# Kernel tuning notes

Hardware: AMD Instinct MI355X
Metric: run time of the kernel (lower is better)

## Reference

```python
import jax, jax.numpy as jnp
import numpy as np

BATCH = 128
SITES = 256      # input_dim, number of MPS input cores
BOND = 64        # bond dimension D
FEAT = 2         # feature_dim
OUT = 10         # output_dim


def setup_inputs() -> dict:
    key = jax.random.key(0)
    k1, k2, k3, k4, k5 = jax.random.split(key, 5)
    # forward input: [batch, input_dim, feature_dim], values in [0,1) like a feature map
    input_data = jax.random.uniform(k1, (BATCH, SITES, FEAT), dtype=jnp.float32)
    # InputRegion core tensor, bond_str 'slri' -> [sites, D, D, feat]
    # small random perturbation; identity bias (use_bias=True, fixed_bias) added in forward
    cores = 0.01 * jax.random.normal(k2, (SITES, BOND, BOND, FEAT), dtype=jnp.float32)
    # OutputSite core, bond_str 'olr' -> [output_dim, D, D]
    out_core = 0.01 * jax.random.normal(k3, (OUT, BOND, BOND), dtype=jnp.float32)
    # boundary (edge) vectors for open boundary conditions
    left_vec = jax.random.normal(k4, (BOND,), dtype=jnp.float32) / np.sqrt(BOND)
    right_vec = jax.random.normal(k5, (BOND,), dtype=jnp.float32) / np.sqrt(BOND)
    return {"input_data": input_data, "cores": cores, "out_core": out_core,
            "left_vec": left_vec, "right_vec": right_vec}


def _chain_matmul(mats):
    """Log-depth product of a chain of matrices. mats: [b, s, D, D] -> [b, D, D].
    Product is ordered: mats[:,0] @ mats[:,1] @ ... @ mats[:,s-1]."""
    b, s, d, _ = mats.shape
    while mats.shape[1] > 1:
        n = mats.shape[1]
        if n % 2 == 1:  # pad with identity so length is even
            eye = jnp.broadcast_to(jnp.eye(d, dtype=mats.dtype), (b, 1, d, d))
            mats = jnp.concatenate([mats, eye], axis=1)
        mats = jnp.matmul(mats[:, 0::2], mats[:, 1::2])
    return mats[:, 0]


def reference(input_data, cores, out_core, left_vec, right_vec):
    # InputRegion.forward: contract each core with its per-site feature vector
    # 'slri,bsi->bslr', then add identity bias matrix (use_bias=True)
    mats = jnp.einsum('slri,bsi->bslr', cores, input_data)
    mats = mats + jnp.eye(BOND, dtype=mats.dtype)  # bias_mat = eye, broadcast over b,s

    # split the chain around the (central) output site, reduce each side
    half = SITES // 2
    left_prod = _chain_matmul(mats[:, :half])    # [b, D, D]
    right_prod = _chain_matmul(mats[:, half:])   # [b, D, D]

    # open-boundary contraction: lvec . Lprod . out_core . Rprod . rvec -> [b, out]
    v = jnp.einsum('l,blr->br', left_vec, left_prod)        # [b, D]
    v = jnp.einsum('bl,olr->bor', v, out_core)              # [b, out, D]
    v = jnp.einsum('bol,blr->bor', v, right_prod)           # [b, out, D]
    logits = jnp.einsum('bor,r->bo', v, right_vec)          # [b, out]
    return logits
```

## Files before the change

kernel.cpp:

```cpp
#include <hip/hip_runtime.h>

#define BOND   64
#define SITES  256
#define HALF   128
#define NBATCH 128
#define OUTD   10

#define P1_OFF   1048576
#define VEC_OFF  2097152
#define SITE_F4  2048
#define LPITCH   132

typedef __attribute__((ext_vector_type(4))) float f32x4;
#define AS1 __attribute__((address_space(1)))
#define AS3 __attribute__((address_space(3)))

__global__ void __launch_bounds__(256)
mps_pack_kernel(const float* __restrict__ cores, float* __restrict__ P) {
  __shared__ __align__(16) float ld[64 * LPITCH];
  const int s = (int)blockIdx.x;
  const int t = (int)threadIdx.x;
  const float4* src = (const float4*)(cores + (size_t)s * 8192);
  #pragma unroll
  for (int k = 0; k < 8; ++k) {
    const int m = t + 256 * k;
    const int row = m >> 5;
    const int c4  = m & 31;
    *(float4*)&ld[row * LPITCH + c4 * 4] = src[m];
  }
  __syncthreads();
  const bool right = s >= HALF;
  const int step = right ? (SITES - 1 - s) : s;
  float4* out = (float4*)(P + (right ? P1_OFF : 0)) + (size_t)step * SITE_F4;
  #pragma unroll
  for (int k = 0; k < 8; ++k) {
    const int m = t + 256 * k;
    const int g = m >> 6;
    const int j = m & 63;
    float4 v;
    if (!right) {
      const float2 a  = *(const float2*)&ld[(2 * g) * LPITCH + 2 * j];
      const float2 b2 = *(const float2*)&ld[(2 * g + 1) * LPITCH + 2 * j];
      v = make_float4(a.x, a.y, b2.x, b2.y);
    } else {
      v = *(const float4*)&ld[j * LPITCH + 4 * g];
    }
    out[m] = v;
  }
}

__device__ __forceinline__ void gload_lds16(const float* g, float* l) {
  __builtin_amdgcn_global_load_lds((const AS1 void*)g, (AS3 void*)l, 16, 0, 0);
}

__global__ void __launch_bounds__(192, 1)
mps_chain_kernel(const float* __restrict__ input,
                 const float* __restrict__ P,
                 const float* __restrict__ lvec,
                 const float* __restrict__ rvec,
                 float* __restrict__ vout) {
  __shared__ __align__(16) float buf0[8192];
  __shared__ __align__(16) float buf1[8192];
  __shared__ __align__(16) float buf2[8192];
  __shared__ __align__(16) float vb[2][68];
  __shared__ __align__(16) float xsh[2][HALF][2];

  const int t    = (int)threadIdx.x;
  const int side = (int)blockIdx.x & 1;
  const int pair = (int)blockIdx.x >> 1;
  const int b0   = 2 * pair;

  if (t < 64) {
    const int lane = t;
    const float* gl = P + (side ? P1_OFF : 0) + lane * 4;
    float* sA = buf0;
    float* sB = buf1;
    float* sC = buf2;
#define STAGEL(LDST, STEPI)                                                  \
    {                                                                        \
      const float* gs = gl + (size_t)(STEPI) * 8192;                         \
      _Pragma("unroll")                                                      \
      for (int k = 0; k < 32; ++k)                                           \
        gload_lds16(gs + k * 256, (LDST) + k * 256);                         \
    }
    STAGEL(sA, 0);
    STAGEL(sB, 1);
    for (int i = 0; i < HALF; ++i) {
      asm volatile("s_waitcnt vmcnt(32)" ::: "memory");
      __builtin_amdgcn_s_barrier();
      const int inx = (i + 2 < HALF) ? i + 2 : HALF - 1;
      STAGEL(sC, inx);
      float* tmp = sA; sA = sB; sB = sC; sC = tmp;
    }
#undef STAGEL
  } else {
    const int tc   = t - 64;
    const int wc   = tc >> 6;
    const int lane = tc & 63;
    const int jcol = (lane >> 1) + 32 * wc;
    const int bs   = lane & 1;

    if (wc == 0) {
      #pragma unroll
      for (int bi = 0; bi < 2; ++bi) {
        const float4 g = ((const float4*)(input + (size_t)(b0 + bi) * SITES * 2 +
                                          side * HALF * 2))[lane];
        float* xw = &xsh[bi][0][0];
        if (!side) {
          ((float4*)xw)[lane] = g;
        } else {
          ((float2*)xw)[HALF - 1 - 2 * lane] = make_float2(g.x, g.y);
          ((float2*)xw)[HALF - 2 - 2 * lane] = make_float2(g.z, g.w);
        }
      }
    }

    float r = side ? rvec[jcol] : lvec[jcol];
    vb[bs][jcol] = r;

    const float* cA = buf0;
    const float* cB = buf1;
    const float* cC = buf2;
    const float* vbp = vb[bs];
    const float* xp  = &xsh[bs][0][0];

    for (int i = 0; i < HALF; ++i) {
      __syncthreads();
      f32x4 vv[16];
      #pragma unroll
      for (int k = 0; k < 16; ++k)
        vv[k] = ((const f32x4*)vbp)[k];
      const float2 xv = *(const float2*)&xp[2 * i];
      float p0a = 0.f, p0b = 0.f, p1a = 0.f, p1b = 0.f;
      #pragma unroll
      for (int q = 0; q < 16; ++q) {
        const f32x4 u  = vv[q];
        const f32x4 mA = *(const f32x4*)&cA[(2 * q) * 256 + jcol * 4];
        const f32x4 mB = *(const f32x4*)&cA[(2 * q + 1) * 256 + jcol * 4];
        p0a = __builtin_fmaf(u.x, mA.x, p0a);
        p1a = __builtin_fmaf(u.x, mA.y, p1a);
        p0b = __builtin_fmaf(u.y, mA.z, p0b);
        p1b = __builtin_fmaf(u.y, mA.w, p1b);
        p0a = __builtin_fmaf(u.z, mB.x, p0a);
        p1a = __builtin_fmaf(u.z, mB.y, p1a);
        p0b = __builtin_fmaf(u.w, mB.z, p0b);
        p1b = __builtin_fmaf(u.w, mB.w, p1b);
      }
      r = __builtin_fmaf(xv.x, p0a + p0b,
          __builtin_fmaf(xv.y, p1a + p1b, r));
      vb[bs][jcol] = r;
      const float* tmp = cA; cA = cB; cB = cC; cC = tmp;
    }

    vout[((size_t)side * NBATCH + b0 + bs) * BOND + jcol] = r;
  }
}

__global__ void __launch_bounds__(64)
mps_combine_kernel(const float* __restrict__ oc,
                   const float* __restrict__ vecs,
                   float* __restrict__ out) {
  __shared__ float vl[BOND];
  const int lane = (int)threadIdx.x;
  const int b = (int)blockIdx.x;
  vl[lane] = vecs[b * BOND + lane];
  const float myvr = vecs[NBATCH * BOND + b * BOND + lane];
  float res[OUTD];
  #pragma unroll
  for (int o = 0; o < OUTD; ++o) {
    float acc = 0.f;
    #pragma unroll
    for (int m = 0; m < BOND; ++m)
      acc = __builtin_fmaf(vl[m], oc[((o * BOND) + m) * BOND + lane], acc);
    acc *= myvr;
    #pragma unroll
    for (int off = 32; off > 0; off >>= 1)
      acc += __shfl_xor(acc, off, 64);
    res[o] = acc;
  }
  if (lane == 0) {
    #pragma unroll
    for (int o = 0; o < OUTD; ++o) out[b * OUTD + o] = res[o];
  }
}

extern "C" void kernel_launch(void* const* d_in, const int* in_sizes, int n_in,
                              void* d_out, int out_size, void* d_ws, size_t ws_size,
                              hipStream_t stream) {
  const float* input = (const float*)d_in[0];
  const float* cores = (const float*)d_in[1];
  const float* oc    = (const float*)d_in[2];
  const float* lvec  = (const float*)d_in[3];
  const float* rvec  = (const float*)d_in[4];
  float* ws  = (float*)d_ws;
  float* out = (float*)d_out;

  hipLaunchKernelGGL(mps_pack_kernel, dim3(SITES), dim3(256), 0, stream,
                     cores, ws);
  hipLaunchKernelGGL(mps_chain_kernel, dim3(NBATCH), dim3(192), 0, stream,
                     input, ws, lvec, rvec, ws + VEC_OFF);
  hipLaunchKernelGGL(mps_combine_kernel, dim3(NBATCH), dim3(64), 0, stream,
                     oc, ws + VEC_OFF, out);
}
```

Before: 147.2 us.

## Split chain matvec reduction across two lane halves with double-buffered vector

```diff
diff --git a/kernel.cpp b/kernel.cpp
--- a/kernel.cpp
+++ b/kernel.cpp
@@ -53,7 +53,7 @@
   __builtin_amdgcn_global_load_lds((const AS1 void*)g, (AS3 void*)l, 16, 0, 0);
 }
 
-__global__ void __launch_bounds__(192, 1)
+__global__ void __launch_bounds__(320, 1)
 mps_chain_kernel(const float* __restrict__ input,
                  const float* __restrict__ P,
                  const float* __restrict__ lvec,
@@ -62,7 +62,7 @@
   __shared__ __align__(16) float buf0[8192];
   __shared__ __align__(16) float buf1[8192];
   __shared__ __align__(16) float buf2[8192];
-  __shared__ __align__(16) float vb[2][68];
+  __shared__ __align__(16) float vbx[2][2][68];
   __shared__ __align__(16) float xsh[2][HALF][2];
 
   const int t    = (int)threadIdx.x;
@@ -94,11 +94,12 @@
     }
 #undef STAGEL
   } else {
-    const int tc   = t - 64;
-    const int wc   = tc >> 6;
-    const int lane = tc & 63;
-    const int jcol = (lane >> 1) + 32 * wc;
-    const int bs   = lane & 1;
+    const int tc    = t - 64;
+    const int wc    = tc >> 6;
+    const int lane  = tc & 63;
+    const int jcol  = (lane & 31) + 32 * (wc & 1);
+    const int bs    = wc >> 1;
+    const int lhalf = lane >> 5;
 
     if (wc == 0) {
       #pragma unroll
@@ -116,43 +117,42 @@
     }
 
     float r = side ? rvec[jcol] : lvec[jcol];
-    vb[bs][jcol] = r;
+    vbx[0][bs][jcol] = r;
 
     const float* cA = buf0;
     const float* cB = buf1;
     const float* cC = buf2;
-    const float* vbp = vb[bs];
-    const float* xp  = &xsh[bs][0][0];
+    const float* xp = &xsh[bs][0][0];
 
     for (int i = 0; i < HALF; ++i) {
       __syncthreads();
-      f32x4 vv[16];
+      const float* vr = &vbx[i & 1][bs][32 * lhalf];
+      f32x4 vv[8];
       #pragma unroll
-      for (int k = 0; k < 16; ++k)
-        vv[k] = ((const f32x4*)vbp)[k];
+      for (int k = 0; k < 8; ++k)
+        vv[k] = ((const f32x4*)vr)[k];
       const float2 xv = *(const float2*)&xp[2 * i];
-      float p0a = 0.f, p0b = 0.f, p1a = 0.f, p1b = 0.f;
+      float p0 = 0.f, p1 = 0.f;
       #pragma unroll
       for (int q = 0; q < 16; ++q) {
-        const f32x4 u  = vv[q];
-        const f32x4 mA = *(const f32x4*)&cA[(2 * q) * 256 + jcol * 4];
-        const f32x4 mB = *(const f32x4*)&cA[(2 * q + 1) * 256 + jcol * 4];
-        p0a = __builtin_fmaf(u.x, mA.x, p0a);
-        p1a = __builtin_fmaf(u.x, mA.y, p1a);
-        p0b = __builtin_fmaf(u.y, mA.z, p0b);
-        p1b = __builtin_fmaf(u.y, mA.w, p1b);
-        p0a = __builtin_fmaf(u.z, mB.x, p0a);
-        p1a = __builtin_fmaf(u.z, mB.y, p1a);
-        p0b = __builtin_fmaf(u.w, mB.z, p0b);
-        p1b = __builtin_fmaf(u.w, mB.w, p1b);
+        const f32x4 m = *(const f32x4*)&cA[(16 * lhalf + q) * 256 + jcol * 4];
+        const f32x4 u = vv[q >> 1];
+        const float va = (q & 1) ? u.z : u.x;
+        const float vb2 = (q & 1) ? u.w : u.y;
+        p0 = __builtin_fmaf(va, m.x, p0);
+        p1 = __builtin_fmaf(va, m.y, p1);
+        p0 = __builtin_fmaf(vb2, m.z, p0);
+        p1 = __builtin_fmaf(vb2, m.w, p1);
       }
-      r = __builtin_fmaf(xv.x, p0a + p0b,
-          __builtin_fmaf(xv.y, p1a + p1b, r));
-      vb[bs][jcol] = r;
+      float tsum = __builtin_fmaf(xv.x, p0, xv.y * p1);
+      tsum += __shfl_xor(tsum, 32, 64);
+      r += tsum;
+      vbx[(i + 1) & 1][bs][jcol] = r;
       const float* tmp = cA; cA = cB; cB = cC; cC = tmp;
     }
 
-    vout[((size_t)side * NBATCH + b0 + bs) * BOND + jcol] = r;
+    if (lhalf == 0)
+      vout[((size_t)side * NBATCH + b0 + bs) * BOND + jcol] = r;
   }
 }
 
@@ -197,7 +197,7 @@
 
   hipLaunchKernelGGL(mps_pack_kernel, dim3(SITES), dim3(256), 0, stream,
                      cores, ws);
-  hipLaunchKernelGGL(mps_chain_kernel, dim3(NBATCH), dim3(192), 0, stream,
+  hipLaunchKernelGGL(mps_chain_kernel, dim3(NBATCH), dim3(320), 0, stream,
                      input, ws, lvec, rvec, ws + VEC_OFF);
   hipLaunchKernelGGL(mps_combine_kernel, dim3(NBATCH), dim3(64), 0, stream,
                      oc, ws + VEC_OFF, out);
```

Measured after the change: 140.2 us. 1.05x faster.
